# Performance work log

Measured on AMD Instinct MI355X. Metric: run time of the kernel, lower is better.

The kernel has to match this reference:

```python
import jax, jax.numpy as jnp
import numpy as np

EPS = 1e-7  # Keras K.epsilon()
ATT_DIM = 50

def setup_inputs() -> dict:
    key = jax.random.key(0)
    k1, k2, k3, k4 = jax.random.split(key, 4)
    B, T, D = 64, 4096, 256
    x = jax.random.normal(k1, (B, T, D), dtype=jnp.float32)
    # RandomNormal init (stddev default 0.05 in keras RandomNormal)
    W = 0.05 * jax.random.normal(k2, (D, ATT_DIM), dtype=jnp.float32)
    b = 0.05 * jax.random.normal(k3, (ATT_DIM,), dtype=jnp.float32)
    u = 0.05 * jax.random.normal(k4, (ATT_DIM, 1), dtype=jnp.float32)
    return {"x": x, "W": W, "b": b, "u": u}

def reference(x, W, b, u):
    # uit: [B, T, A]
    uit = jnp.tanh(jnp.einsum('btd,da->bta', x, W) + b)
    # ait: [B, T]  (no max-subtraction, faithful to K.exp then normalize)
    ait = jnp.exp(jnp.einsum('bta,a->bt', uit, u[:, 0]))
    ait = ait / (jnp.sum(ait, axis=1, keepdims=True) + EPS)
    # weighted sum pooling over seq axis -> [B, D]
    return jnp.einsum('btd,bt->bd', x, ait)
```

## Files before the change

kernel.cpp:

```cpp
#include <hip/hip_runtime.h>
#include <stdint.h>

#define B_    64
#define T_    4096
#define D_    256
#define A_    50
#define APAD  64
#define TB    256
#define ST    32
#define WT_STRIDE 264
#define XS_STRIDE 264
#define EPS_  1e-7f

#define OFF_NUM 0
#define OFF_DEN 16384
#define OFF_B   16448
#define OFF_U   16512
#define OFF_WT  16576

typedef __attribute__((ext_vector_type(8))) short short8;
typedef __attribute__((ext_vector_type(4))) float floatx4;

__device__ __forceinline__ unsigned short f32_to_bf16(float f) {
    union { float f; uint32_t u; } v; v.f = f;
    uint32_t u = v.u;
    uint32_t r = u + 0x7FFFu + ((u >> 16) & 1u);
    return (unsigned short)(r >> 16);
}

__device__ __forceinline__ float fast_tanh(float x) {
    float e2 = __expf(2.0f * x);
    return (e2 - 1.0f) * __builtin_amdgcn_rcpf(e2 + 1.0f);
}

__global__ void att_prologue(const float* __restrict__ W,
                             const float* __restrict__ bias,
                             const float* __restrict__ u,
                             float* __restrict__ ws) {
    int idx = blockIdx.x * blockDim.x + threadIdx.x;
    int stride = gridDim.x * blockDim.x;
    for (int i = idx; i < OFF_DEN + B_; i += stride) ws[i] = 0.0f;
    for (int i = idx; i < APAD; i += stride) {
        ws[OFF_B + i] = (i < A_) ? bias[i] : 0.0f;
        ws[OFF_U + i] = (i < A_) ? u[i]    : 0.0f;
    }
    unsigned short* wt = (unsigned short*)(ws + OFF_WT);
    for (int i = idx; i < APAD * D_; i += stride) {
        int a = i >> 8;
        int k = i & 255;
        float val = (a < A_) ? W[k * A_ + a] : 0.0f;
        wt[a * WT_STRIDE + k] = f32_to_bf16(val);
    }
}

__global__ __launch_bounds__(256, 4) void att_main(const float* __restrict__ x,
                                                   float* __restrict__ ws) {
    __shared__ unsigned short lds_x[ST * XS_STRIDE];
    __shared__ float part[ST][4];
    __shared__ float e_lds[ST];

    const int tid  = threadIdx.x;
    const int wave = tid >> 6;
    const int lane = tid & 63;
    const int bb   = blockIdx.y;
    const int tblk = blockIdx.x;

    const float* xblk = x + ((size_t)bb * T_ + (size_t)tblk * TB) * D_;

    float4 r[8];
    {
        const float4* xg = (const float4*)xblk;
        #pragma unroll
        for (int i = 0; i < 4; ++i) {
            r[2 * i]     = xg[2 * tid + 512 * i];
            r[2 * i + 1] = xg[2 * tid + 512 * i + 1];
        }
    }

    short8 bw[8];
    {
        const unsigned short* wt = (const unsigned short*)(ws + OFF_WT);
        const unsigned short* wrow = wt + (wave * 16 + (lane & 15)) * WT_STRIDE
                                        + ((lane >> 4) * 8);
        #pragma unroll
        for (int ks = 0; ks < 8; ++ks)
            bw[ks] = *(const short8*)(wrow + ks * 32);
    }

    const int c = wave * 16 + (lane & 15);
    const float b_c = ws[OFF_B + c];
    const float u_c = ws[OFF_U + c];

    float num_acc = 0.0f;
    float den_acc = 0.0f;

    const int arow0 = (lane & 15) * XS_STRIDE;
    const int arow1 = (16 + (lane & 15)) * XS_STRIDE;
    const int koff  = (lane >> 4) * 8;
    const int wrow_lds = (tid >> 5) * XS_STRIDE + (tid & 31) * 8;

    for (int st = 0; st < TB / ST; ++st) {
        __syncthreads();

        #pragma unroll
        for (int i = 0; i < 4; ++i) {
            uint4 p;
            p.x = ((uint32_t)f32_to_bf16(r[2*i].y)   << 16) | f32_to_bf16(r[2*i].x);
            p.y = ((uint32_t)f32_to_bf16(r[2*i].w)   << 16) | f32_to_bf16(r[2*i].z);
            p.z = ((uint32_t)f32_to_bf16(r[2*i+1].y) << 16) | f32_to_bf16(r[2*i+1].x);
            p.w = ((uint32_t)f32_to_bf16(r[2*i+1].w) << 16) | f32_to_bf16(r[2*i+1].z);
            *(uint4*)&lds_x[wrow_lds + i * 8 * XS_STRIDE] = p;
        }
        __syncthreads();

        if (st < TB / ST - 1) {
            const float4* xn = (const float4*)(xblk + (st + 1) * ST * D_);
            #pragma unroll
            for (int i = 0; i < 4; ++i) {
                r[2 * i]     = xn[2 * tid + 512 * i];
                r[2 * i + 1] = xn[2 * tid + 512 * i + 1];
            }
        }

        floatx4 acc0 = {0.f, 0.f, 0.f, 0.f};
        floatx4 acc1 = {0.f, 0.f, 0.f, 0.f};
        #pragma unroll
        for (int ks = 0; ks < 8; ++ks) {
            short8 a0 = *(const short8*)&lds_x[arow0 + ks * 32 + koff];
            short8 a1 = *(const short8*)&lds_x[arow1 + ks * 32 + koff];
            acc0 = __builtin_amdgcn_mfma_f32_16x16x32_bf16(a0, bw[ks], acc0, 0, 0, 0);
            acc1 = __builtin_amdgcn_mfma_f32_16x16x32_bf16(a1, bw[ks], acc1, 0, 0, 0);
        }

        float lp0[4], lp1[4];
        #pragma unroll
        for (int rr = 0; rr < 4; ++rr) {
            float v0 = fast_tanh(acc0[rr] + b_c) * u_c;
            float v1 = fast_tanh(acc1[rr] + b_c) * u_c;
            v0 += __shfl_xor(v0, 1); v1 += __shfl_xor(v1, 1);
            v0 += __shfl_xor(v0, 2); v1 += __shfl_xor(v1, 2);
            v0 += __shfl_xor(v0, 4); v1 += __shfl_xor(v1, 4);
            v0 += __shfl_xor(v0, 8); v1 += __shfl_xor(v1, 8);
            lp0[rr] = v0; lp1[rr] = v1;
        }
        if ((lane & 15) == 0) {
            int rg = lane >> 4;
            #pragma unroll
            for (int rr = 0; rr < 4; ++rr) {
                part[rg * 4 + rr][wave]      = lp0[rr];
                part[16 + rg * 4 + rr][wave] = lp1[rr];
            }
        }
        __syncthreads();

        if (tid < ST) {
            float ev = __expf(part[tid][0] + part[tid][1] + part[tid][2] + part[tid][3]);
            e_lds[tid] = ev;
            den_acc += ev;
        }
        __syncthreads();

        #pragma unroll
        for (int t = 0; t < ST; ++t) {
            float xv = __uint_as_float((uint32_t)lds_x[t * XS_STRIDE + tid] << 16);
            num_acc = fmaf(xv, e_lds[t], num_acc);
        }
    }

    atomicAdd(&ws[OFF_NUM + bb * D_ + tid], num_acc);
    if (wave == 0) {
        float v = den_acc;
        v += __shfl_xor(v, 32);
        v += __shfl_xor(v, 16);
        v += __shfl_xor(v, 8);
        v += __shfl_xor(v, 4);
        v += __shfl_xor(v, 2);
        v += __shfl_xor(v, 1);
        if (lane == 0) atomicAdd(&ws[OFF_DEN + bb], v);
    }
}

__global__ void att_epilogue(const float* __restrict__ ws, float* __restrict__ out) {
    int bb = blockIdx.x;
    int d  = threadIdx.x;
    out[bb * D_ + d] = ws[OFF_NUM + bb * D_ + d] / (ws[OFF_DEN + bb] + EPS_);
}

extern "C" void kernel_launch(void* const* d_in, const int* in_sizes, int n_in,
                              void* d_out, int out_size, void* d_ws, size_t ws_size,
                              hipStream_t stream) {
    const float* x = (const float*)d_in[0];
    const float* W = (const float*)d_in[1];
    const float* b = (const float*)d_in[2];
    const float* u = (const float*)d_in[3];
    float* ws  = (float*)d_ws;
    float* out = (float*)d_out;

    att_prologue<<<64, 256, 0, stream>>>(W, b, u, ws);
    att_main<<<dim3(T_ / TB, B_), 256, 0, stream>>>(x, ws);
    att_epilogue<<<B_, 256, 0, stream>>>(ws, out);
}
```

Before: 366.7 us.

## Accumulate pooled sum in fp32 registers and replace atomics with partial buffers

The weighted-sum pooling now uses the fp32 x values still held in registers, with double-buffered register sets (rA/rB), instead of re-reading bf16 values from LDS per time step. Each block reduces its per-thread partials through LDS and writes them to a per-block partial slot, and the epilogue sums those slots. This replaces the global atomics and the zero-init in the prologue. Global loads use nontemporal hints, and launch bounds drop to 3 blocks per CU to make room for the larger register footprint, at the cost of occupancy.

```diff
diff --git a/kernel.cpp b/kernel.cpp
--- a/kernel.cpp
+++ b/kernel.cpp
@@ -8,15 +8,16 @@
 #define APAD  64
 #define TB    256
 #define ST    32
+#define NSUB  (TB / ST)
 #define WT_STRIDE 264
 #define XS_STRIDE 264
 #define EPS_  1e-7f
 
-#define OFF_NUM 0
-#define OFF_DEN 16384
-#define OFF_B   16448
-#define OFF_U   16512
-#define OFF_WT  16576
+#define OFF_B   0
+#define OFF_U   64
+#define OFF_WT  128
+#define OFF_NP  (OFF_WT + 8448)
+#define OFF_DP  (OFF_NP + 64*16*256)
 
 typedef __attribute__((ext_vector_type(8))) short short8;
 typedef __attribute__((ext_vector_type(4))) float floatx4;
@@ -39,7 +40,6 @@
                              float* __restrict__ ws) {
     int idx = blockIdx.x * blockDim.x + threadIdx.x;
     int stride = gridDim.x * blockDim.x;
-    for (int i = idx; i < OFF_DEN + B_; i += stride) ws[i] = 0.0f;
     for (int i = idx; i < APAD; i += stride) {
         ws[OFF_B + i] = (i < A_) ? bias[i] : 0.0f;
         ws[OFF_U + i] = (i < A_) ? u[i]    : 0.0f;
@@ -53,7 +53,7 @@
     }
 }
 
-__global__ __launch_bounds__(256, 4) void att_main(const float* __restrict__ x,
+__global__ __launch_bounds__(256, 3) void att_main(const float* __restrict__ x,
                                                    float* __restrict__ ws) {
     __shared__ unsigned short lds_x[ST * XS_STRIDE];
     __shared__ float part[ST][4];
@@ -67,13 +67,13 @@
 
     const float* xblk = x + ((size_t)bb * T_ + (size_t)tblk * TB) * D_;
 
-    float4 r[8];
-    {
-        const float4* xg = (const float4*)xblk;
+    floatx4 rA[8], rB[8];
+    {
+        const floatx4* xg = (const floatx4*)xblk;
         #pragma unroll
         for (int i = 0; i < 4; ++i) {
-            r[2 * i]     = xg[2 * tid + 512 * i];
-            r[2 * i + 1] = xg[2 * tid + 512 * i + 1];
+            rA[2*i]   = __builtin_nontemporal_load(&xg[2*tid + 512*i]);
+            rA[2*i+1] = __builtin_nontemporal_load(&xg[2*tid + 512*i + 1]);
         }
     }
 
@@ -91,34 +91,35 @@
     const float b_c = ws[OFF_B + c];
     const float u_c = ws[OFF_U + c];
 
-    float num_acc = 0.0f;
+    float num_part[8] = {0.f,0.f,0.f,0.f,0.f,0.f,0.f,0.f};
     float den_acc = 0.0f;
 
     const int arow0 = (lane & 15) * XS_STRIDE;
     const int arow1 = (16 + (lane & 15)) * XS_STRIDE;
     const int koff  = (lane >> 4) * 8;
     const int wrow_lds = (tid >> 5) * XS_STRIDE + (tid & 31) * 8;
-
-    for (int st = 0; st < TB / ST; ++st) {
+    const int erow = tid >> 5;
+
+    auto body = [&](int st, floatx4 (&rc)[8], floatx4 (&rn)[8]) {
         __syncthreads();
 
         #pragma unroll
         for (int i = 0; i < 4; ++i) {
             uint4 p;
-            p.x = ((uint32_t)f32_to_bf16(r[2*i].y)   << 16) | f32_to_bf16(r[2*i].x);
-            p.y = ((uint32_t)f32_to_bf16(r[2*i].w)   << 16) | f32_to_bf16(r[2*i].z);
-            p.z = ((uint32_t)f32_to_bf16(r[2*i+1].y) << 16) | f32_to_bf16(r[2*i+1].x);
-            p.w = ((uint32_t)f32_to_bf16(r[2*i+1].w) << 16) | f32_to_bf16(r[2*i+1].z);
+            p.x = ((uint32_t)f32_to_bf16(rc[2*i][1])   << 16) | f32_to_bf16(rc[2*i][0]);
+            p.y = ((uint32_t)f32_to_bf16(rc[2*i][3])   << 16) | f32_to_bf16(rc[2*i][2]);
+            p.z = ((uint32_t)f32_to_bf16(rc[2*i+1][1]) << 16) | f32_to_bf16(rc[2*i+1][0]);
+            p.w = ((uint32_t)f32_to_bf16(rc[2*i+1][3]) << 16) | f32_to_bf16(rc[2*i+1][2]);
             *(uint4*)&lds_x[wrow_lds + i * 8 * XS_STRIDE] = p;
         }
         __syncthreads();
 
-        if (st < TB / ST - 1) {
-            const float4* xn = (const float4*)(xblk + (st + 1) * ST * D_);
+        if (st + 1 < NSUB) {
+            const floatx4* xn = (const floatx4*)(xblk + (st + 1) * ST * D_);
             #pragma unroll
             for (int i = 0; i < 4; ++i) {
-                r[2 * i]     = xn[2 * tid + 512 * i];
-                r[2 * i + 1] = xn[2 * tid + 512 * i + 1];
+                rn[2*i]   = __builtin_nontemporal_load(&xn[2*tid + 512*i]);
+                rn[2*i+1] = __builtin_nontemporal_load(&xn[2*tid + 512*i + 1]);
             }
         }
 
@@ -161,13 +162,36 @@
         __syncthreads();
 
         #pragma unroll
-        for (int t = 0; t < ST; ++t) {
-            float xv = __uint_as_float((uint32_t)lds_x[t * XS_STRIDE + tid] << 16);
-            num_acc = fmaf(xv, e_lds[t], num_acc);
-        }
-    }
-
-    atomicAdd(&ws[OFF_NUM + bb * D_ + tid], num_acc);
+        for (int i = 0; i < 4; ++i) {
+            float ev = e_lds[erow + 8 * i];
+            #pragma unroll
+            for (int j = 0; j < 4; ++j) {
+                num_part[j]     = fmaf(rc[2*i][j],   ev, num_part[j]);
+                num_part[4 + j] = fmaf(rc[2*i+1][j], ev, num_part[4 + j]);
+            }
+        }
+    };
+
+    #pragma unroll
+    for (int k = 0; k < NSUB; k += 2) {
+        body(k,     rA, rB);
+        body(k + 1, rB, rA);
+    }
+
+    __syncthreads();
+    float* red = (float*)lds_x;
+    {
+        int g = tid >> 5, cc = (tid & 31) * 8;
+        *(floatx4*)&red[g * 264 + cc]     = (floatx4){num_part[0], num_part[1], num_part[2], num_part[3]};
+        *(floatx4*)&red[g * 264 + cc + 4] = (floatx4){num_part[4], num_part[5], num_part[6], num_part[7]};
+    }
+    __syncthreads();
+    {
+        float s = 0.0f;
+        #pragma unroll
+        for (int g = 0; g < 8; ++g) s += red[g * 264 + tid];
+        ws[OFF_NP + ((size_t)bb * 16 + tblk) * 256 + tid] = s;
+    }
     if (wave == 0) {
         float v = den_acc;
         v += __shfl_xor(v, 32);
@@ -176,14 +200,20 @@
         v += __shfl_xor(v, 4);
         v += __shfl_xor(v, 2);
         v += __shfl_xor(v, 1);
-        if (lane == 0) atomicAdd(&ws[OFF_DEN + bb], v);
+        if (lane == 0) ws[OFF_DP + bb * 16 + tblk] = v;
     }
 }
 
 __global__ void att_epilogue(const float* __restrict__ ws, float* __restrict__ out) {
     int bb = blockIdx.x;
     int d  = threadIdx.x;
-    out[bb * D_ + d] = ws[OFF_NUM + bb * D_ + d] / (ws[OFF_DEN + bb] + EPS_);
+    float num = 0.0f, den = 0.0f;
+    #pragma unroll
+    for (int k = 0; k < 16; ++k) {
+        num += ws[OFF_NP + ((size_t)bb * 16 + k) * 256 + d];
+        den += ws[OFF_DP + bb * 16 + k];
+    }
+    out[bb * D_ + d] = num / (den + EPS_);
 }
 
 extern "C" void kernel_launch(void* const* d_in, const int* in_sizes, int n_in,
@@ -196,7 +226,7 @@
     float* ws  = (float*)d_ws;
     float* out = (float*)d_out;
 
-    att_prologue<<<64, 256, 0, stream>>>(W, b, u, ws);
+    att_prologue<<<32, 256, 0, stream>>>(W, b, u, ws);
     att_main<<<dim3(T_ / TB, B_), 256, 0, stream>>>(x, ws);
     att_epilogue<<<B_, 256, 0, stream>>>(ws, out);
 }
```

After: 441.0 us. 20.3% more time.
